# Performance work log

Hardware: AMD Instinct MI355X
Metric: run time of the kernel (lower is better)

## Reference

```python
import jax, jax.numpy as jnp
import numpy as np

NUM_HEADS = 8
NEG_INF = -1e30


def _within_bucket_rank(idx):
    # idx: [U] int32 bucket ids; returns occurrence count of each id among earlier positions
    U = idx.shape[0]
    order = jnp.argsort(idx, stable=True)
    sv = idx[order]
    pos = jnp.arange(U, dtype=jnp.int32)
    is_start = jnp.concatenate([jnp.ones((1,), bool), sv[1:] != sv[:-1]])
    start = jax.lax.cummax(jnp.where(is_start, pos, 0))
    rank = pos - start
    return jnp.zeros(U, jnp.int32).at[order].set(rank)


def setup_inputs() -> dict:
    key = jax.random.key(0)
    ks = jax.random.split(key, 10)
    B, U, G, E = 8, 16384, 64, 128
    lin = jnp.linspace(0.0, 1.0, G)
    gx, gy = jnp.meshgrid(lin, lin, indexing='ij')
    xc_on_grid = jnp.broadcast_to(jnp.stack([gx, gy], -1), (B, G, G, 2)).astype(jnp.float32)
    s = 0.02
    return {
        'xc_off_grid': jax.random.uniform(ks[0], (B, U, 2), jnp.float32),
        'xc_on_grid': xc_on_grid,
        'zc_off_grid': jax.random.normal(ks[1], (B, U, E), jnp.float32),
        'zc_on_grid': jax.random.normal(ks[2], (B, G, G, E), jnp.float32),
        'latents': jax.random.normal(ks[3], (G * G, E), jnp.float32),
        'fake_embedding': jax.random.normal(ks[4], (E,), jnp.float32),
        'Wq': jax.random.normal(ks[5], (E, E), jnp.float32) * s,
        'Wk': jax.random.normal(ks[6], (E, E), jnp.float32) * s,
        'Wv': jax.random.normal(ks[7], (E, E), jnp.float32) * s,
        'Wo': jax.random.normal(ks[8], (E, E), jnp.float32) * s,
        'ignore_on_grid': 0,
    }


def _bucketize(xc_off_grid, xc_on_grid):
    # returns nearest flat grid index per off-grid point, shape [B, U] int32
    B = xc_off_grid.shape[0]
    dims = xc_on_grid.shape[1:-1]
    S = int(np.prod(dims))
    grid_shape = jnp.asarray(dims, jnp.float32)
    x_on = xc_on_grid.reshape(B, S, -1)
    xmin = x_on.min(axis=(0, 1))
    xmax = x_on.max(axis=(0, 1))
    spacing = (xmax - xmin) / (grid_shape - 1.0)
    nm = jnp.floor((xc_off_grid - xmin + spacing / 2) / spacing)
    nm = jnp.clip(nm, 0.0, grid_shape - 1.0)
    # strides as in the original: flip(cumprod([1, *dims])[:-1])
    strides = np.flip(np.cumprod(np.concatenate([[1], np.asarray(dims)]))[:-1]).astype(np.float32)
    return (nm * jnp.asarray(strides)).sum(-1).astype(jnp.int32)


def _mhca(latents_q, kv, valid, Wq, Wk, Wv, Wo):
    # latents_q: [N,1,E], kv: [N,P,E], valid: [N,P] bool
    N, P, E = kv.shape
    H, Dh = NUM_HEADS, E // NUM_HEADS
    q = (latents_q @ Wq).reshape(N, 1, H, Dh)
    k = (kv @ Wk).reshape(N, P, H, Dh)
    v = (kv @ Wv).reshape(N, P, H, Dh)
    scores = jnp.einsum('nqhd,nkhd->nhqk', q, k) / jnp.sqrt(jnp.asarray(Dh, q.dtype))
    scores = jnp.where(valid[:, None, None, :], scores, NEG_INF)
    attn = jax.nn.softmax(scores, axis=-1)
    out = jnp.einsum('nhqk,nkhd->nqhd', attn, v).reshape(N, 1, E)
    return out @ Wo


def reference(xc_off_grid, xc_on_grid, zc_off_grid, zc_on_grid, latents, fake_embedding, Wq, Wk, Wv, Wo, ignore_on_grid):
    B, U, E = zc_off_grid.shape
    dims = xc_on_grid.shape[1:-1]
    S = int(np.prod(dims))
    z_on = zc_on_grid.reshape(B, S, E)

    nearest_idx = _bucketize(xc_off_grid, xc_on_grid)          # [B, U]
    cumcount = jax.vmap(_within_bucket_rank)(nearest_idx)       # [B, U]
    flat_seg = (nearest_idx + jnp.arange(B, dtype=jnp.int32)[:, None] * S).reshape(-1)
    counts = jax.ops.segment_sum(jnp.ones(B * U, jnp.int32), flat_seg, num_segments=B * S)
    max_patch = int(jax.device_get(counts.max())) + 1           # +1 slot for on-grid/fake token

    # ragged scatter of off-grid tokens into padded per-bucket buffer
    grid_stacked = jnp.zeros((B * S, max_patch, E), zc_off_grid.dtype)
    grid_stacked = grid_stacked.at[flat_seg, cumcount.reshape(-1)].set(zc_off_grid.reshape(B * U, E))
    if ignore_on_grid:
        last = jnp.broadcast_to(fake_embedding, (B * S, E))
    else:
        last = z_on.reshape(B * S, E)
    grid_stacked = grid_stacked.at[:, -1].set(last)

    slot = jnp.arange(max_patch)
    valid = (slot[None, :] < counts[:, None]) | (slot[None, :] == max_patch - 1)  # [B*S, P]

    lat = jnp.broadcast_to(latents[None], (B, S, E)).reshape(B * S, 1, E)
    zc = _mhca(lat, grid_stacked, valid, Wq, Wk, Wv, Wo)        # [B*S, 1, E]
    return zc.reshape(B, *dims, E)
```

## Files before the change

kernel.cpp:

```cpp
#include <hip/hip_runtime.h>
#include <hip/hip_bf16.h>
#include <math.h>

namespace {
constexpr int B_  = 8;
constexpr int U_  = 16384;
constexpr int S_  = 4096;
constexpr int E_  = 128;
constexpr int NTOK  = B_ * U_;
constexpr int NCELL = B_ * S_;
constexpr int FUSED_GRID = 1024;
constexpr int CAP = 32;
constexpr int SWZ2 = 2 * 16384;
}

typedef __attribute__((ext_vector_type(8))) short bf16x8;
typedef __attribute__((ext_vector_type(4))) float f32x4;

__device__ inline unsigned short bf16rne(float x) {
  unsigned u = __float_as_uint(x);
  u = u + 0x7fffu + ((u >> 16) & 1u);
  return (unsigned short)(u >> 16);
}

__device__ inline bf16x8 pack8(float4 a, float4 b) {
  union { __hip_bfloat162 h; unsigned int u; } q0, q1, q2, q3;
  q0.h = __float22bfloat162_rn(make_float2(a.x, a.y));
  q1.h = __float22bfloat162_rn(make_float2(a.z, a.w));
  q2.h = __float22bfloat162_rn(make_float2(b.x, b.y));
  q3.h = __float22bfloat162_rn(make_float2(b.z, b.w));
  union { unsigned int u[4]; bf16x8 v; } r;
  r.u[0] = q0.u; r.u[1] = q1.u; r.u[2] = q2.u; r.u[3] = q3.u;
  return r.v;
}

__global__ __launch_bounds__(1024, 4) void setup_kernel(
    const float* __restrict__ Wq, const float* __restrict__ Wk,
    const float* __restrict__ Wv, const float* __restrict__ Wo,
    const float* __restrict__ latents, const float* __restrict__ xc_off,
    unsigned short* __restrict__ Wsw, unsigned short* __restrict__ QKt,
    int* __restrict__ cnt, int* __restrict__ sorted) {
  const int tid = threadIdx.x;

  if (blockIdx.x < 128) {
    __shared__ __align__(16) unsigned short wq[16384];
    __shared__ float wkt[128 * 129];
    __shared__ float qbuf[32 * 128];
    const int s0 = blockIdx.x * 32;

    for (int i = tid; i < 16384; i += 1024) {
      const int k = i >> 7, n = i & 127;
      wq[(((k >> 3) * 128 + n) << 3) + (k & 7)] = bf16rne(Wq[i]);
      wkt[(i & 127) * 129 + (i >> 7)] = Wk[i];
    }
    __syncthreads();

    const int wave = tid >> 6, lane = tid & 63;
    const int c = lane & 15, g = lane >> 4;
    if (wave < 2) {
      const int t0w = s0 + wave * 16;
      f32x4 acc[8];
#pragma unroll
      for (int i = 0; i < 8; ++i) acc[i] = {0.f, 0.f, 0.f, 0.f};
      const float* arow = latents + (size_t)(t0w + c) * E_ + g * 8;
      const bf16x8* bq = (const bf16x8*)wq;
#pragma unroll
      for (int ks = 0; ks < 4; ++ks) {
        float4 a0 = *(const float4*)(arow + ks * 32);
        float4 a1 = *(const float4*)(arow + ks * 32 + 4);
        bf16x8 af = pack8(a0, a1);
        const int bo = (ks * 4 + g) * 128 + c;
#pragma unroll
        for (int nt = 0; nt < 8; ++nt)
          acc[nt] = __builtin_amdgcn_mfma_f32_16x16x32_bf16(af, bq[bo + nt * 16], acc[nt], 0, 0, 0);
      }
#pragma unroll
      for (int nt = 0; nt < 8; ++nt)
#pragma unroll
        for (int r = 0; r < 4; ++r)
          qbuf[(wave * 16 + g * 4 + r) * 128 + nt * 16 + c] = acc[nt][r] * 0.25f;
    }
    __syncthreads();

#pragma unroll
    for (int k = 0; k < 32; ++k) {
      const int o = k * 1024 + tid;
      const int e = o & 127, h = (o >> 7) & 7, sl = o >> 10;
      float acc = 0.f;
#pragma unroll
      for (int j = 0; j < 16; ++j)
        acc = fmaf(wkt[(h * 16 + j) * 129 + e], qbuf[sl * 128 + h * 16 + j], acc);
      QKt[(size_t)(s0 + sl) * 1024 + (e >> 3) * 64 + h * 8 + (e & 7)] = bf16rne(acc);
    }
  } else {
    const int base = (blockIdx.x - 128) * 1024 + tid;
    const int stride = 128 * 1024;
    for (int i = base; i < SWZ2 + NTOK; i += stride) {
      if (i < SWZ2) {
        const int w = i >> 14, e = i & 16383;
        const int k = e >> 7, n = e & 127;
        const float* src = (w == 0) ? Wv : Wo;
        Wsw[w * 16384 + (((k >> 3) * 128 + n) << 3) + (k & 7)] = bf16rne(src[e]);
      } else {
        const int tok = i - SWZ2;
        const int b = tok >> 14;
        const float sp = 1.0f / 63.0f;
        const float half = sp * 0.5f;
        const float x0 = xc_off[(size_t)tok * 2 + 0];
        const float x1 = xc_off[(size_t)tok * 2 + 1];
        float n0 = floorf((x0 - 0.0f + half) / sp);
        float n1 = floorf((x1 - 0.0f + half) / sp);
        n0 = fminf(fmaxf(n0, 0.0f), 63.0f);
        n1 = fminf(fmaxf(n1, 0.0f), 63.0f);
        const int seg = b * S_ + (int)(n0 * 64.0f + n1);
        const int rank = atomicAdd(&cnt[seg], 1);
        if (rank < CAP) sorted[seg * CAP + rank] = tok;
      }
    }
  }
}

__global__ __launch_bounds__(512, 4) void fused_cells(
    const float* __restrict__ zc_off, const float* __restrict__ zc_on,
    const float* __restrict__ fake, const int* __restrict__ ignore_flag,
    const unsigned short* __restrict__ Wv_sw,
    const unsigned short* __restrict__ QKt, const int* __restrict__ cnt,
    const int* __restrict__ sorted, float* __restrict__ out) {
  __shared__ __align__(16) unsigned short wv[16384];
  __shared__ float wbuf[8][16][9];
  const int tid = threadIdx.x;
  {
    const uint4* sv = (const uint4*)Wv_sw;
    uint4* dv = (uint4*)wv;
#pragma unroll
    for (int i = 0; i < 4; ++i) dv[i * 512 + tid] = sv[i * 512 + tid];
  }
  const int ign = *ignore_flag;
  __syncthreads();

  const int wave = tid >> 6, lane = tid & 63;
  const int c = lane & 15, g = lane >> 4;
  const bf16x8* bv = (const bf16x8*)wv;

  for (int grp = blockIdx.x; grp < NCELL / 8; grp += FUSED_GRID) {
    const int cell = grp * 8 + wave;
    const int s = cell & (S_ - 1);
    const int base = cell * CAP;
    const int n_off = min(cnt[cell], CAP);
    const bf16x8* bqk = (const bf16x8*)(QKt + (size_t)s * 1024);

    float num_acc[8], den_acc[8];
#pragma unroll
    for (int i = 0; i < 8; ++i) { num_acc[i] = 0.f; den_acc[i] = 0.f; }

    const int chunks = (n_off + 16) >> 4;

    for (int ch = 0; ch < chunks; ++ch) {
      const int idx = ch * 16 + c;
      const float* arow;
      if (idx < n_off)       arow = zc_off + (size_t)sorted[base + idx] * E_;
      else if (idx == n_off) arow = ign ? fake : (zc_on + (size_t)cell * E_);
      else                   arow = zc_on;
      arow += g * 8;

      bf16x8 af[4];
#pragma unroll
      for (int ks = 0; ks < 4; ++ks) {
        float4 a0 = *(const float4*)(arow + ks * 32);
        float4 a1 = *(const float4*)(arow + ks * 32 + 4);
        af[ks] = pack8(a0, a1);
      }

      f32x4 aS = {0.f, 0.f, 0.f, 0.f};
#pragma unroll
      for (int ks = 0; ks < 4; ++ks)
        aS = __builtin_amdgcn_mfma_f32_16x16x32_bf16(af[ks], bqk[(ks * 4 + g) * 8 + (c & 7)], aS, 0, 0, 0);

      if (c < 8) {
#pragma unroll
        for (int r = 0; r < 4; ++r) {
          const int t = g * 4 + r;
          wbuf[wave][t][c] = (ch * 16 + t <= n_off) ? __expf(aS[r]) : 0.f;
        }
      }

#pragma unroll 2
      for (int h = 0; h < 8; ++h) {
        float wr[4];
#pragma unroll
        for (int r = 0; r < 4; ++r) wr[r] = wbuf[wave][g * 4 + r][h];

        const int bo = g * 128 + c + h * 16;
        f32x4 aV = {0.f, 0.f, 0.f, 0.f};
#pragma unroll
        for (int ks = 0; ks < 4; ++ks)
          aV = __builtin_amdgcn_mfma_f32_16x16x32_bf16(af[ks], bv[bo + ks * 512], aV, 0, 0, 0);

        float sv = 0.f, sd = 0.f;
#pragma unroll
        for (int r = 0; r < 4; ++r) { sv = fmaf(wr[r], aV[r], sv); sd += wr[r]; }
        num_acc[h] += sv;
        den_acc[h] += sd;
      }
    }

#pragma unroll
    for (int i = 0; i < 8; ++i) {
      num_acc[i] += __shfl_xor(num_acc[i], 16, 64);
      num_acc[i] += __shfl_xor(num_acc[i], 32, 64);
      den_acc[i] += __shfl_xor(den_acc[i], 16, 64);
      den_acc[i] += __shfl_xor(den_acc[i], 32, 64);
    }
#pragma unroll
    for (int b = 0; b < 2; ++b) {
      const int nt = 2 * g + b;
      out[(size_t)cell * E_ + nt * 16 + c] = num_acc[nt] / den_acc[nt];
    }
  }
}

__global__ __launch_bounds__(512, 4) void finalize_mfma(
    const unsigned short* __restrict__ Wo_sw, float* __restrict__ out) {
  __shared__ __align__(16) unsigned short wo[16384];
  const int tid = threadIdx.x;
  {
    const uint4* s = (const uint4*)Wo_sw;
    uint4* d = (uint4*)wo;
#pragma unroll
    for (int i = 0; i < 4; ++i) d[i * 512 + tid] = s[i * 512 + tid];
  }
  __syncthreads();

  const int wave = tid >> 6, lane = tid & 63;
  const int c = lane & 15, g = lane >> 4;
  const int t0w = blockIdx.x * 128 + wave * 16;

  f32x4 acc[8];
#pragma unroll
  for (int i = 0; i < 8; ++i) acc[i] = {0.f, 0.f, 0.f, 0.f};

  const float* nrow = out + (size_t)(t0w + c) * E_ + g * 8;
  const bf16x8* bo_ = (const bf16x8*)wo;
#pragma unroll
  for (int ks = 0; ks < 4; ++ks) {
    float4 a0 = *(const float4*)(nrow + ks * 32);
    float4 a1 = *(const float4*)(nrow + ks * 32 + 4);
    bf16x8 af = pack8(a0, a1);
    const int bofs = (ks * 4 + g) * 128 + c;
#pragma unroll
    for (int nt = 0; nt < 8; ++nt)
      acc[nt] = __builtin_amdgcn_mfma_f32_16x16x32_bf16(af, bo_[bofs + nt * 16], acc[nt], 0, 0, 0);
  }
#pragma unroll
  for (int nt = 0; nt < 8; ++nt)
#pragma unroll
    for (int r = 0; r < 4; ++r)
      out[(size_t)(t0w + g * 4 + r) * E_ + nt * 16 + c] = acc[nt][r];
}

extern "C" void kernel_launch(void* const* d_in, const int* in_sizes, int n_in,
                              void* d_out, int out_size, void* d_ws, size_t ws_size,
                              hipStream_t stream) {
  const float* xc_off  = (const float*)d_in[0];
  const float* zc_off  = (const float*)d_in[2];
  const float* zc_on   = (const float*)d_in[3];
  const float* latents = (const float*)d_in[4];
  const float* fake    = (const float*)d_in[5];
  const float* Wq      = (const float*)d_in[6];
  const float* Wk      = (const float*)d_in[7];
  const float* Wv      = (const float*)d_in[8];
  const float* Wo      = (const float*)d_in[9];
  const int*   ignore  = (const int*)d_in[10];

  float* out = (float*)d_out;

  unsigned short* QKt = (unsigned short*)d_ws;
  unsigned short* Wsw = QKt + (size_t)S_ * 1024;
  int* cnt    = (int*)(Wsw + SWZ2);
  int* sorted = cnt + NCELL;
  unsigned short* Wv_sw = Wsw;
  unsigned short* Wo_sw = Wsw + 16384;

  hipMemsetAsync(cnt, 0, NCELL * sizeof(int), stream);
  setup_kernel<<<256, 1024, 0, stream>>>(Wq, Wk, Wv, Wo, latents, xc_off,
                                         Wsw, QKt, cnt, sorted);
  fused_cells<<<FUSED_GRID, 512, 0, stream>>>(zc_off, zc_on, fake, ignore,
                                              Wv_sw, QKt, cnt, sorted, out);
  finalize_mfma<<<NCELL / 128, 512, 0, stream>>>(Wo_sw, out);
}
```

Measured before the change: 186.1 us.

## Pack two cells per wave into each 16-row MFMA tile

Each wave now handles two adjacent cells, giving each cell 8 rows of the 16-row MFMA tile instead of one cell per 16-row chunk. Cells typically hold only a few off-grid tokens plus one on-grid token, so the old layout left most rows as padding. The new layout is meant to cut wasted MFMA work and global loads on padding rows and halve the number of loop iterations per cell. In exchange it adds per-half indexing logic, and a chunk now runs as long as the larger count of the two cells.

```diff
diff --git a/kernel.cpp b/kernel.cpp
--- a/kernel.cpp
+++ b/kernel.cpp
@@ -140,27 +140,33 @@
 
   const int wave = tid >> 6, lane = tid & 63;
   const int c = lane & 15, g = lane >> 4;
+  const int half = c >> 3;
+  const int hwr  = g >> 1;
   const bf16x8* bv = (const bf16x8*)wv;
 
-  for (int grp = blockIdx.x; grp < NCELL / 8; grp += FUSED_GRID) {
-    const int cell = grp * 8 + wave;
-    const int s = cell & (S_ - 1);
-    const int base = cell * CAP;
-    const int n_off = min(cnt[cell], CAP);
-    const bf16x8* bqk = (const bf16x8*)(QKt + (size_t)s * 1024);
+  for (int grp = blockIdx.x; grp < NCELL / 16; grp += FUSED_GRID) {
+    const int slot = grp * 8 + wave;
+    const int cA = slot * 2, cB = cA + 1;
+    const int sA = cA & (S_ - 1);
+    const int nA = min(cnt[cA], CAP);
+    const int nB = min(cnt[cB], CAP);
+    const int cH = half ? cB : cA;
+    const int nH = half ? nB : nA;
+    const int baseH = cH * CAP;
+    const bf16x8* bqk = (const bf16x8*)(QKt + (size_t)(sA + half) * 1024);
 
     float num_acc[8], den_acc[8];
 #pragma unroll
     for (int i = 0; i < 8; ++i) { num_acc[i] = 0.f; den_acc[i] = 0.f; }
 
-    const int chunks = (n_off + 16) >> 4;
+    const int chunks = max((nA + 8) >> 3, (nB + 8) >> 3);
 
     for (int ch = 0; ch < chunks; ++ch) {
-      const int idx = ch * 16 + c;
+      const int jj = ch * 8 + (c & 7);
       const float* arow;
-      if (idx < n_off)       arow = zc_off + (size_t)sorted[base + idx] * E_;
-      else if (idx == n_off) arow = ign ? fake : (zc_on + (size_t)cell * E_);
-      else                   arow = zc_on;
+      if (jj < nH)       arow = zc_off + (size_t)sorted[baseH + jj] * E_;
+      else if (jj == nH) arow = ign ? fake : (zc_on + (size_t)cH * E_);
+      else               arow = zc_on;
       arow += g * 8;
 
       bf16x8 af[4];
@@ -176,11 +182,12 @@
       for (int ks = 0; ks < 4; ++ks)
         aS = __builtin_amdgcn_mfma_f32_16x16x32_bf16(af[ks], bqk[(ks * 4 + g) * 8 + (c & 7)], aS, 0, 0, 0);
 
-      if (c < 8) {
+      if (hwr == half) {
 #pragma unroll
         for (int r = 0; r < 4; ++r) {
           const int t = g * 4 + r;
-          wbuf[wave][t][c] = (ch * 16 + t <= n_off) ? __expf(aS[r]) : 0.f;
+          const int jt = ch * 8 + (t & 7);
+          wbuf[wave][t][c & 7] = (jt <= nH) ? __expf(aS[r]) : 0.f;
         }
       }
 
@@ -207,14 +214,14 @@
 #pragma unroll
     for (int i = 0; i < 8; ++i) {
       num_acc[i] += __shfl_xor(num_acc[i], 16, 64);
-      num_acc[i] += __shfl_xor(num_acc[i], 32, 64);
       den_acc[i] += __shfl_xor(den_acc[i], 16, 64);
-      den_acc[i] += __shfl_xor(den_acc[i], 32, 64);
-    }
-#pragma unroll
-    for (int b = 0; b < 2; ++b) {
-      const int nt = 2 * g + b;
-      out[(size_t)cell * E_ + nt * 16 + c] = num_acc[nt] / den_acc[nt];
+    }
+    const int cellO = hwr ? cB : cA;
+    const int hb = (g & 1) * 4;
+#pragma unroll
+    for (int b = 0; b < 4; ++b) {
+      const int h = hb + b;
+      out[(size_t)cellO * E_ + h * 16 + c] = num_acc[h] / den_acc[h];
     }
   }
 }
```

New measurement: 177.2 us. 4.8% less time.
